# Kernel tuning notes

Hardware: AMD Instinct MI355X
Metric: run time of the kernel (lower is better)

Reference implementation:

```python
import jax, jax.numpy as jnp
import numpy as np

# loss hyperparams (from init_kwargs / KeypointsMSESmoothLoss defaults in source)
SCALE_KPS = 0.1
THRESHOLD = 100.0
ALPHA = 0.1
BETA = 0.9

B, V, J = 8192, 8, 32


def setup_inputs() -> dict:
    key = jax.random.key(0)
    k1, k2, k3, k4 = jax.random.split(key, 4)
    # realistic pinhole intrinsics, broadcast per batch/view
    f, cx, cy = 1500.0, 500.0, 500.0
    K_base = jnp.array([[f, 0.0, cx], [0.0, f, cy], [0.0, 0.0, 1.0]], jnp.float32)
    K = jnp.broadcast_to(K_base, (B, V, 3, 3)) + 0.01 * jax.random.normal(k1, (B, V, 3, 3), jnp.float32)
    # camera extrinsics [R|t]; push t_z positive so points sit in front of camera
    cam_preds = 0.1 * jax.random.normal(k2, (B, V, 3, 4), jnp.float32)
    cam_preds = cam_preds.at[..., 2, 3].add(10.0)
    kps_world_pred = jax.random.normal(k3, (B, J, 3), jnp.float32)
    initial_keypoints = 100.0 * jax.random.normal(k4, (B, V, J, 2), jnp.float32)
    return {"K": K, "cam_preds": cam_preds, "kps_world_pred": kps_world_pred,
            "initial_keypoints": initial_keypoints}


def reference(K, cam_preds, kps_world_pred, initial_keypoints):
    b, v = cam_preds.shape[0], cam_preds.shape[1]
    # project_to_weak_views: world -> camera -> image, perspective divide
    ones = jnp.ones_like(kps_world_pred[..., :1])
    Xh = jnp.concatenate([kps_world_pred, ones], axis=-1)          # [B,J,4]
    cam_pts = jnp.einsum('bvij,bnj->bvni', cam_preds, Xh)          # [B,V,J,3]
    img_pts = jnp.einsum('bvij,bvnj->bvni', K, cam_pts)            # [B,V,J,3]
    proj = img_pts[..., :2] / img_pts[..., 2:3]                    # [B,V,J,2]
    # penalization: |fro_norm(proj)/fro_norm(init) - 1| per (batch, view)
    pn = jnp.linalg.norm(proj.reshape(b, v, -1), axis=-1)
    inorm = jnp.linalg.norm(initial_keypoints.reshape(b, v, -1), axis=-1)
    penal = jnp.abs(pn / inorm - 1.0)                              # [B,V]
    # KeypointsMSESmoothLoss on scaled keypoints (no validity mask)
    diff = ((proj - initial_keypoints) * SCALE_KPS) ** 2           # [B,V,J,2]
    over = diff > THRESHOLD
    safe = jnp.where(over, diff, THRESHOLD)
    diff = jnp.where(over, safe ** ALPHA * THRESHOLD ** BETA, diff)
    per_view_loss = diff.sum(axis=(-1, -2)) / 2.0                  # dimension = last dim = 2
    return jnp.mean(per_view_loss * penal)
```

## Files before the change

kernel.cpp:

```cpp
#include <hip/hip_runtime.h>
#include <math.h>

#define B_TOT 8192
#define V_N 8
#define J_N 32

#define SCALE_KPS 0.1f
#define THRESH 100.0f
#define THRESH_BETA 63.09573444801932f

__device__ __forceinline__ float smooth_term(float d) {
    return (d > THRESH)
        ? __builtin_amdgcn_exp2f(0.1f * __builtin_amdgcn_logf(d)) * THRESH_BETA
        : d;
}

__global__ __launch_bounds__(256) void qpl_fused(
    const float* __restrict__ Kmat,
    const float* __restrict__ cam,
    const float* __restrict__ kps,
    const float* __restrict__ init,
    float* __restrict__ partial)
{
    __shared__ float s_acc[4];

    const int tid  = threadIdx.x;
    const int wave = tid >> 6;
    const int lane = tid & 63;
    const int v    = lane >> 3;
    const int t    = lane & 7;
    const int b    = blockIdx.x * 4 + wave;

    const float4* kp4 = (const float4*)(kps + (size_t)b * (J_N * 3) + t * 12);
    const float4 f0 = kp4[0], f1 = kp4[1], f2 = kp4[2];

    const float* cv = cam + (size_t)b * (V_N * 12) + v * 12;
    const float4 c0 = ((const float4*)cv)[0];
    const float4 c1 = ((const float4*)cv)[1];
    const float4 c2 = ((const float4*)cv)[2];

    const float* kv = Kmat + (size_t)b * (V_N * 9) + v * 9;
    const float k0 = kv[0], k1 = kv[1], k2 = kv[2];
    const float k3 = kv[3], k4 = kv[4], k5 = kv[5];
    const float k6 = kv[6], k7 = kv[7], k8 = kv[8];

    const float4* ib = (const float4*)(init + (size_t)b * (V_N * J_N * 2) + lane * 8);
    const float4 q0 = ib[0], q1 = ib[1];

    const float xs[4]  = {f0.x, f0.w, f1.z, f2.y};
    const float ys[4]  = {f0.y, f1.x, f1.w, f2.z};
    const float zs[4]  = {f0.z, f1.y, f2.x, f2.w};
    const float ikx[4] = {q0.x, q0.z, q1.x, q1.z};
    const float iky[4] = {q0.y, q0.w, q1.y, q1.w};

    float sum_diff = 0.0f, sum_p2 = 0.0f, sum_i2 = 0.0f;

    #pragma unroll
    for (int m = 0; m < 4; ++m) {
        const float cp0 = c0.x * xs[m] + c0.y * ys[m] + c0.z * zs[m] + c0.w;
        const float cp1 = c1.x * xs[m] + c1.y * ys[m] + c1.z * zs[m] + c1.w;
        const float cp2 = c2.x * xs[m] + c2.y * ys[m] + c2.z * zs[m] + c2.w;

        const float i0 = k0 * cp0 + k1 * cp1 + k2 * cp2;
        const float i1 = k3 * cp0 + k4 * cp1 + k5 * cp2;
        const float i2 = k6 * cp0 + k7 * cp1 + k8 * cp2;

        const float r  = __builtin_amdgcn_rcpf(i2);
        const float p0 = i0 * r;
        const float p1 = i1 * r;

        float d0 = (p0 - ikx[m]) * SCALE_KPS; d0 *= d0;
        float d1 = (p1 - iky[m]) * SCALE_KPS; d1 *= d1;

        sum_diff += smooth_term(d0) + smooth_term(d1);
        sum_p2   += p0 * p0 + p1 * p1;
        sum_i2   += ikx[m] * ikx[m] + iky[m] * iky[m];
    }

    #pragma unroll
    for (int m = 1; m <= 4; m <<= 1) {
        sum_diff += __shfl_xor(sum_diff, m);
        sum_p2   += __shfl_xor(sum_p2, m);
        sum_i2   += __shfl_xor(sum_i2, m);
    }

    const float penal = fabsf(sqrtf(sum_p2 * __builtin_amdgcn_rcpf(sum_i2)) - 1.0f);
    float acc = (sum_diff * 0.5f) * penal;

    acc += __shfl_xor(acc, 8);
    acc += __shfl_xor(acc, 16);
    acc += __shfl_xor(acc, 32);

    if (lane == 0) s_acc[wave] = acc;
    __syncthreads();
    if (tid == 0)
        partial[blockIdx.x] = s_acc[0] + s_acc[1] + s_acc[2] + s_acc[3];
}

__global__ __launch_bounds__(256) void qpl_reduce(
    const float* __restrict__ partial, float* __restrict__ out)
{
    __shared__ float s_w[4];
    float t = 0.0f;
    #pragma unroll
    for (int k = 0; k < 8; ++k) t += partial[threadIdx.x + k * 256];

    #pragma unroll
    for (int m = 32; m >= 1; m >>= 1) t += __shfl_xor(t, m);

    if ((threadIdx.x & 63) == 0) s_w[threadIdx.x >> 6] = t;
    __syncthreads();

    if (threadIdx.x == 0) {
        const float tot = s_w[0] + s_w[1] + s_w[2] + s_w[3];
        out[0] = tot * (1.0f / (float)(B_TOT * V_N));
    }
}

extern "C" void kernel_launch(void* const* d_in, const int* in_sizes, int n_in,
                              void* d_out, int out_size, void* d_ws, size_t ws_size,
                              hipStream_t stream) {
    const float* Kmat = (const float*)d_in[0];
    const float* cam  = (const float*)d_in[1];
    const float* kps  = (const float*)d_in[2];
    const float* init = (const float*)d_in[3];
    float* partial = (float*)d_ws;
    float* out     = (float*)d_out;

    qpl_fused<<<B_TOT / 4, 256, 0, stream>>>(Kmat, cam, kps, init, partial);
    qpl_reduce<<<1, 256, 0, stream>>>(partial, out);
}
```

Before: 77.72 us.

## Fuse final reduction via last-block atomic counter and premultiply K·[R|t]

Replaces the separate reduction kernel with a last-block-done pattern: each block stores its partial sum, bumps an atomic counter, and the final block sums all partials and writes the mean. The intrinsics and extrinsics are premultiplied into one 3x4 matrix per view, so each keypoint needs fewer FMAs. Launch bounds now request higher occupancy. In exchange it adds a hipMemsetAsync for the counter, fences and an atomic per block.

```diff
diff --git a/kernel.cpp b/kernel.cpp
--- a/kernel.cpp
+++ b/kernel.cpp
@@ -4,6 +4,7 @@
 #define B_TOT 8192
 #define V_N 8
 #define J_N 32
+#define GRID_N (B_TOT / 4)
 
 #define SCALE_KPS 0.1f
 #define THRESH 100.0f
@@ -15,14 +16,17 @@
         : d;
 }
 
-__global__ __launch_bounds__(256) void qpl_fused(
+__global__ __launch_bounds__(256, 8) void qpl_fused(
     const float* __restrict__ Kmat,
     const float* __restrict__ cam,
     const float* __restrict__ kps,
     const float* __restrict__ init,
-    float* __restrict__ partial)
+    float* __restrict__ partial,
+    unsigned int* __restrict__ counter,
+    float* __restrict__ out)
 {
     __shared__ float s_acc[4];
+    __shared__ unsigned int s_old;
 
     const int tid  = threadIdx.x;
     const int wave = tid >> 6;
@@ -30,9 +34,6 @@
     const int v    = lane >> 3;
     const int t    = lane & 7;
     const int b    = blockIdx.x * 4 + wave;
-
-    const float4* kp4 = (const float4*)(kps + (size_t)b * (J_N * 3) + t * 12);
-    const float4 f0 = kp4[0], f1 = kp4[1], f2 = kp4[2];
 
     const float* cv = cam + (size_t)b * (V_N * 12) + v * 12;
     const float4 c0 = ((const float4*)cv)[0];
@@ -44,8 +45,19 @@
     const float k3 = kv[3], k4 = kv[4], k5 = kv[5];
     const float k6 = kv[6], k7 = kv[7], k8 = kv[8];
 
+    const float4* kp4 = (const float4*)(kps + (size_t)b * (J_N * 3) + t * 12);
+    const float4 f0 = kp4[0], f1 = kp4[1], f2 = kp4[2];
+
     const float4* ib = (const float4*)(init + (size_t)b * (V_N * J_N * 2) + lane * 8);
     const float4 q0 = ib[0], q1 = ib[1];
+
+    float4 m0, m1, m2;
+    m0.x = k0*c0.x + k1*c1.x + k2*c2.x;  m0.y = k0*c0.y + k1*c1.y + k2*c2.y;
+    m0.z = k0*c0.z + k1*c1.z + k2*c2.z;  m0.w = k0*c0.w + k1*c1.w + k2*c2.w;
+    m1.x = k3*c0.x + k4*c1.x + k5*c2.x;  m1.y = k3*c0.y + k4*c1.y + k5*c2.y;
+    m1.z = k3*c0.z + k4*c1.z + k5*c2.z;  m1.w = k3*c0.w + k4*c1.w + k5*c2.w;
+    m2.x = k6*c0.x + k7*c1.x + k8*c2.x;  m2.y = k6*c0.y + k7*c1.y + k8*c2.y;
+    m2.z = k6*c0.z + k7*c1.z + k8*c2.z;  m2.w = k6*c0.w + k7*c1.w + k8*c2.w;
 
     const float xs[4]  = {f0.x, f0.w, f1.z, f2.y};
     const float ys[4]  = {f0.y, f1.x, f1.w, f2.z};
@@ -57,13 +69,9 @@
 
     #pragma unroll
     for (int m = 0; m < 4; ++m) {
-        const float cp0 = c0.x * xs[m] + c0.y * ys[m] + c0.z * zs[m] + c0.w;
-        const float cp1 = c1.x * xs[m] + c1.y * ys[m] + c1.z * zs[m] + c1.w;
-        const float cp2 = c2.x * xs[m] + c2.y * ys[m] + c2.z * zs[m] + c2.w;
-
-        const float i0 = k0 * cp0 + k1 * cp1 + k2 * cp2;
-        const float i1 = k3 * cp0 + k4 * cp1 + k5 * cp2;
-        const float i2 = k6 * cp0 + k7 * cp1 + k8 * cp2;
+        const float i0 = m0.w + m0.x * xs[m] + m0.y * ys[m] + m0.z * zs[m];
+        const float i1 = m1.w + m1.x * xs[m] + m1.y * ys[m] + m1.z * zs[m];
+        const float i2 = m2.w + m2.x * xs[m] + m2.y * ys[m] + m2.z * zs[m];
 
         const float r  = __builtin_amdgcn_rcpf(i2);
         const float p0 = i0 * r;
@@ -93,28 +101,33 @@
 
     if (lane == 0) s_acc[wave] = acc;
     __syncthreads();
-    if (tid == 0)
-        partial[blockIdx.x] = s_acc[0] + s_acc[1] + s_acc[2] + s_acc[3];
-}
 
-__global__ __launch_bounds__(256) void qpl_reduce(
-    const float* __restrict__ partial, float* __restrict__ out)
-{
-    __shared__ float s_w[4];
-    float t = 0.0f;
+    if (tid == 0) {
+        const float bs = s_acc[0] + s_acc[1] + s_acc[2] + s_acc[3];
+        __hip_atomic_store(&partial[blockIdx.x], bs,
+                           __ATOMIC_RELAXED, __HIP_MEMORY_SCOPE_AGENT);
+        __threadfence();
+        s_old = __hip_atomic_fetch_add(counter, 1u,
+                                       __ATOMIC_ACQ_REL, __HIP_MEMORY_SCOPE_AGENT);
+    }
+    __syncthreads();
+    if (s_old != GRID_N - 1) return;
+
+    __threadfence();
+    float tsum = 0.0f;
     #pragma unroll
-    for (int k = 0; k < 8; ++k) t += partial[threadIdx.x + k * 256];
+    for (int k = 0; k < GRID_N / 256; ++k)
+        tsum += __hip_atomic_load(&partial[tid + k * 256],
+                                  __ATOMIC_RELAXED, __HIP_MEMORY_SCOPE_AGENT);
 
     #pragma unroll
-    for (int m = 32; m >= 1; m >>= 1) t += __shfl_xor(t, m);
+    for (int m = 32; m >= 1; m >>= 1) tsum += __shfl_xor(tsum, m);
 
-    if ((threadIdx.x & 63) == 0) s_w[threadIdx.x >> 6] = t;
+    if (lane == 0) s_acc[wave] = tsum;
     __syncthreads();
-
-    if (threadIdx.x == 0) {
-        const float tot = s_w[0] + s_w[1] + s_w[2] + s_w[3];
-        out[0] = tot * (1.0f / (float)(B_TOT * V_N));
-    }
+    if (tid == 0)
+        out[0] = (s_acc[0] + s_acc[1] + s_acc[2] + s_acc[3])
+               * (1.0f / (float)(B_TOT * V_N));
 }
 
 extern "C" void kernel_launch(void* const* d_in, const int* in_sizes, int n_in,
@@ -125,8 +138,9 @@
     const float* kps  = (const float*)d_in[2];
     const float* init = (const float*)d_in[3];
     float* partial = (float*)d_ws;
-    float* out     = (float*)d_out;
+    unsigned int* counter = (unsigned int*)((char*)d_ws + GRID_N * sizeof(float));
+    float* out = (float*)d_out;
 
-    qpl_fused<<<B_TOT / 4, 256, 0, stream>>>(Kmat, cam, kps, init, partial);
-    qpl_reduce<<<1, 256, 0, stream>>>(partial, out);
+    hipMemsetAsync(counter, 0, sizeof(unsigned int), stream);
+    qpl_fused<<<GRID_N, 256, 0, stream>>>(Kmat, cam, kps, init, partial, counter, out);
 }
```

Result: slower. 161.9 us (+108.3%).
